# Optimization experiments

Hardware: AMD Instinct MI355X
Metric: run time of the kernel (lower is better)

## Reference

```python
import jax, jax.numpy as jnp
import numpy as np

N_HEADS = 4
N_HIDDEN = 512  # out_features with concat=False
SLOPE = 0.01
NEG = -1e9


def setup_inputs() -> dict:
    key = jax.random.key(0)
    k1, k2, k3, k4 = jax.random.split(key, 4)
    N, F_IN = 8192, 512
    h = jax.random.normal(k1, (N, F_IN), dtype=jnp.float32)
    W = jax.random.normal(k2, (F_IN, N_HIDDEN * N_HEADS), dtype=jnp.float32) * 0.05
    a = jax.random.normal(k3, (N_HEADS, 2 * N_HIDDEN, 1), dtype=jnp.float32) * 0.05
    adj_mat = jnp.where(jax.random.uniform(k4, (N, N)) < 0.01, 0.0, NEG).astype(jnp.float32)
    return {"h": h, "adj_mat": adj_mat, "W": W, "a": a}


def reference(h, adj_mat, W, a):
    N = h.shape[0]
    # [N, H*d] -> [H, N, d]
    ht = (h @ W).reshape(N, N_HEADS, N_HIDDEN).transpose(1, 0, 2)
    a_src = a[:, :N_HIDDEN, 0]   # [H, d]
    a_dst = a[:, N_HIDDEN:, 0]   # [H, d]
    src = jnp.einsum('hnd,hd->hn', ht, a_src)  # [H, N]
    dst = jnp.einsum('hnd,hd->hn', ht, a_dst)  # [H, N]
    # e[h,i,j] = leaky_relu(src[h,i] + dst[h,j]) + adj_mat[i,j]
    e = jax.nn.leaky_relu(src[:, :, None] + dst[:, None, :], SLOPE) + adj_mat[None]
    att = jax.nn.softmax(e, axis=-1)           # [H, N, N]
    h_prime = jnp.einsum('hij,hjd->hid', att, ht)  # [H, N, d]
    return h_prime.mean(axis=0)                # concat=False -> head mean, [N, d]
```

## Files before the change

### kernel.cpp

```cpp
#include <hip/hip_runtime.h>
#include <stdint.h>

#define NN 8192
#define DH 512
#define NH 4
#define LOG2E 1.4426950408889634f

typedef __attribute__((ext_vector_type(8))) short short8;
typedef __attribute__((ext_vector_type(4))) float f32x4;

__device__ __forceinline__ unsigned short f2bf(float f) {
    unsigned int u = __float_as_uint(f);
    unsigned int r = (u + 0x7fffu + ((u >> 16) & 1u)) >> 16;
    return (unsigned short)r;
}

__device__ __forceinline__ void global_to_lds16(const void* g, void* l) {
    __builtin_amdgcn_global_load_lds(
        (const __attribute__((address_space(1))) unsigned int*)g,
        (__attribute__((address_space(3))) unsigned int*)l, 16, 0, 0);
}

__global__ void k_convert_h(const float* __restrict__ hf, unsigned short* __restrict__ hb) {
    const int idx = (blockIdx.x * 256 + threadIdx.x) * 8;
    const float4 f0 = *(const float4*)(hf + idx);
    const float4 f1 = *(const float4*)(hf + idx + 4);
    uint4 o;
    o.x = (unsigned)f2bf(f0.x) | ((unsigned)f2bf(f0.y) << 16);
    o.y = (unsigned)f2bf(f0.z) | ((unsigned)f2bf(f0.w) << 16);
    o.z = (unsigned)f2bf(f1.x) | ((unsigned)f2bf(f1.y) << 16);
    o.w = (unsigned)f2bf(f1.z) | ((unsigned)f2bf(f1.w) << 16);
    *(uint4*)(hb + idx) = o;
}

__global__ void k_transpose_W(const float* __restrict__ W, unsigned short* __restrict__ Wt) {
    __shared__ float t[32][33];
    const int tx = threadIdx.x & 31, ty = threadIdx.x >> 5;
    const int p0 = blockIdx.x * 32, k0 = blockIdx.y * 32;
#pragma unroll
    for (int r = 0; r < 4; r++)
        t[ty + r * 8][tx] = W[(k0 + ty + r * 8) * 2048 + p0 + tx];
    __syncthreads();
#pragma unroll
    for (int r = 0; r < 4; r++)
        Wt[(size_t)(p0 + ty + r * 8) * 512 + k0 + tx] = f2bf(t[tx][ty + r * 8]);
}

__global__ __launch_bounds__(256, 3) void k_gemm(const unsigned short* __restrict__ Wt,
                                                 const unsigned short* __restrict__ hb,
                                                 unsigned short* __restrict__ vt,
                                                 const float* __restrict__ a,
                                                 float* __restrict__ srcL,
                                                 float* __restrict__ dstL) {
    __shared__ alignas(16) char smem[32768];
    const int tid = threadIdx.x;
    const int w = tid >> 6, lane = tid & 63;
    const int lr = lane & 15, lc = lane >> 4;
    const int pBase = blockIdx.y * 128, nBase = blockIdx.x * 128;
    f32x4 acc[4][4] = {};
    const int wr = (w >> 1) * 64, wc = (w & 1) * 64;
    for (int kb = 0; kb < 8; kb++) {
        const int k0 = kb * 64;
#pragma unroll
        for (int it = 0; it < 4; it++) {
            const int o = it * 4096 + w * 1024 + lane * 16;
            const int row = o >> 7;
            const int koff = (o & 127) >> 1;
            global_to_lds16(Wt + (size_t)(pBase + row) * 512 + k0 + koff,
                            smem + it * 4096 + w * 1024);
            global_to_lds16(hb + (size_t)(nBase + row) * 512 + k0 + koff,
                            smem + 16384 + it * 4096 + w * 1024);
        }
        __syncthreads();
#pragma unroll
        for (int kk = 0; kk < 2; kk++) {
            short8 av[4], bv[4];
#pragma unroll
            for (int m = 0; m < 4; m++)
                av[m] = *(const short8*)(smem + (wr + m * 16 + lr) * 128 + kk * 64 + lc * 16);
#pragma unroll
            for (int n = 0; n < 4; n++)
                bv[n] = *(const short8*)(smem + 16384 + (wc + n * 16 + lr) * 128 + kk * 64 + lc * 16);
#pragma unroll
            for (int m = 0; m < 4; m++)
#pragma unroll
                for (int n = 0; n < 4; n++)
                    acc[m][n] = __builtin_amdgcn_mfma_f32_16x16x32_bf16(av[m], bv[n], acc[m][n], 0, 0, 0);
        }
        __syncthreads();
    }
#pragma unroll
    for (int m = 0; m < 4; m++)
#pragma unroll
        for (int n = 0; n < 4; n++)
#pragma unroll
            for (int q = 0; q < 4; q++) {
                const int p = pBase + wr + m * 16 + lc * 4 + q;
                const int ncol = nBase + wc + n * 16 + lr;
                vt[(size_t)p * NN + ncol] = f2bf(acc[m][n][q]);
            }
    const int hh = pBase >> 9;
    const float* __restrict__ ah = a + hh * 1024;
    float ssum[4] = {0.f, 0.f, 0.f, 0.f}, tsum[4] = {0.f, 0.f, 0.f, 0.f};
#pragma unroll
    for (int m = 0; m < 4; m++) {
        const int dbase = (pBase & 511) + wr + m * 16 + lc * 4;
#pragma unroll
        for (int q = 0; q < 4; q++) {
            const float as = ah[dbase + q];
            const float ad = ah[512 + dbase + q];
#pragma unroll
            for (int n = 0; n < 4; n++) {
                ssum[n] += acc[m][n][q] * as;
                tsum[n] += acc[m][n][q] * ad;
            }
        }
    }
#pragma unroll
    for (int n = 0; n < 4; n++) {
        ssum[n] += __shfl_xor(ssum[n], 16, 64);
        ssum[n] += __shfl_xor(ssum[n], 32, 64);
        tsum[n] += __shfl_xor(tsum[n], 16, 64);
        tsum[n] += __shfl_xor(tsum[n], 32, 64);
    }
    if (lane < 16) {
#pragma unroll
        for (int n = 0; n < 4; n++) {
            const int ncol = nBase + wc + n * 16 + lane;
            __hip_atomic_fetch_add(&srcL[hh * NN + ncol], ssum[n] * LOG2E,
                                   __ATOMIC_RELAXED, __HIP_MEMORY_SCOPE_AGENT);
            __hip_atomic_fetch_add(&dstL[hh * NN + ncol], tsum[n] * LOG2E,
                                   __ATOMIC_RELAXED, __HIP_MEMORY_SCOPE_AGENT);
        }
    }
}

#define NJT (NN / 32)
__global__ __launch_bounds__(512, 2) void k_flash(const float* __restrict__ adj,
                                                  const unsigned short* __restrict__ vt,
                                                  const float* __restrict__ srcL,
                                                  const float* __restrict__ dstL,
                                                  float* __restrict__ out) {
    __shared__ alignas(16) char smem[163840];
    char* const vb0 = smem;
    char* const vb1 = smem + 32768;
    char* const vb2 = smem + 65536;
    char* const ab0 = smem + 98304;
    char* const ab1 = smem + 114688;
    char* const ab2 = smem + 131072;
    char* const pb0 = smem + 147456;
    char* const pb1 = smem + 155648;
    float* denom = (float*)(smem + 98304);

    const int tid = threadIdx.x;
    const int w = tid >> 6, lane = tid & 63;
    const int lr = lane & 15, lc = lane >> 4;
    const int h = (int)(blockIdx.x >> 6);
    const int i0 = (int)(blockIdx.x & 63) * 128;
    const int ih = w >> 2, dq = w & 3;

    const int srow = i0 + w * 16 + lr;
    const float srcv = srcL[h * NN + srow];
    const float* __restrict__ dlp = dstL + h * NN + lc * 8;
    const unsigned short* __restrict__ vth = vt + (size_t)(h * 512) * NN;
    float dsum = 0.f;
    f32x4 acc[4][8] = {};

    unsigned voff[4];
#pragma unroll
    for (int it = 0; it < 4; it++) {
        const int o = it * 8192 + w * 1024 + lane * 16;
        const int row = o >> 7;
        const int z = ((o >> 4) & 7) ^ (row & 7);
        const int d = (row << 1) | (z >> 2);
        voff[it] = (unsigned)d * NN + ((z & 3) << 3);
    }
    unsigned aoff[2];
#pragma unroll
    for (int it = 0; it < 2; it++) {
        const int o = it * 8192 + w * 1024 + lane * 16;
        const int row = o >> 7;
        const int hc = ((o >> 4) & 7) ^ (row & 7);
        aoff[it] = (unsigned)(i0 + row) * NN + hc * 4;
    }
    const int rladj = w * 16 + lr;
    const int g1 = (2 * lc) ^ (lr & 7);
    const int ar1 = rladj * 128 + (g1 << 4);
    const int ar2 = rladj * 128 + ((g1 ^ 1) << 4);
    const int prow = w * 16 + lr;
    const int psl = (((prow & 1) << 2) | lc) ^ ((prow >> 1) & 7);
    const int poff = (prow >> 1) * 128 + (psl << 4);

#define STAGE(J0, DST)                                                                   \
    {                                                                                    \
        _Pragma("unroll") for (int it = 0; it < 4; it++)                                 \
            global_to_lds16(vth + voff[it] + (J0), (DST) + it * 8192 + w * 1024);        \
    }

#define STAGE_ADJ(J0, DST)                                                               \
    {                                                                                    \
        _Pragma("unroll") for (int it = 0; it < 2; it++)                                 \
            global_to_lds16(adj + aoff[it] + (J0), (DST) + it * 8192 + w * 1024);        \
    }

#define SCORE(AR_, J0)                                                                   \
    {                                                                                    \
        const float4 aj0 = *(const float4*)((AR_) + ar1);                                \
        const float4 aj1 = *(const float4*)((AR_) + ar2);                                \
        const float padj[8] = {aj0.x, aj0.y, aj0.z, aj0.w, aj1.x, aj1.y, aj1.z, aj1.w};  \
        const float pdst[8] = {dlA0.x, dlA0.y, dlA0.z, dlA0.w,                           \
                               dlA1.x, dlA1.y, dlA1.z, dlA1.w};                          \
        float pv[8];                                                                     \
        _Pragma("unroll") for (int q = 0; q < 8; q++) {                                  \
            const float x = srcv + pdst[q];                                              \
            const float l2 = fmaxf(x, 0.01f * x);                                        \
            float e;                                                                     \
            asm("v_exp_f32 %0, %1" : "=v"(e) : "v"(l2 + padj[q]));                       \
            dsum += e;                                                                   \
            pv[q] = e;                                                                   \
        }                                                                                \
        union { unsigned u[4]; short8 s; } pk;                                           \
        asm("v_cvt_pk_bf16_f32 %0, %1, %2" : "=v"(pk.u[0]) : "v"(pv[0]), "v"(pv[1]));    \
        asm("v_cvt_pk_bf16_f32 %0, %1, %2" : "=v"(pk.u[1]) : "v"(pv[2]), "v"(pv[3]));    \
        asm("v_cvt_pk_bf16_f32 %0, %1, %2" : "=v"(pk.u[2]) : "v"(pv[4]), "v"(pv[5]));    \
        asm("v_cvt_pk_bf16_f32 %0, %1, %2" : "=v"(pk.u[3]) : "v"(pv[6]), "v"(pv[7]));    \
        pfrag = pk.s;                                                                    \
    }

#define PV(VBUF, PBUF)                                                                   \
    {                                                                                    \
        const char* vbp = (VBUF);                                                        \
        const char* pbp = (PBUF);                                                        \
        short8 afr[4];                                                                   \
        _Pragma("unroll") for (int t = 0; t < 4; t++) {                                  \
            const int rr = ih * 64 + t * 16 + lr;                                        \
            const int sl = (((rr & 1) << 2) | lc) ^ ((rr >> 1) & 7);                     \
            afr[t] = *(const short8*)(pbp + (rr >> 1) * 128 + (sl << 4));                \
        }                                                                                \
        __builtin_amdgcn_s_setprio(1);                                                   \
        _Pragma("unroll") for (int s = 0; s < 8; s++) {                                  \
            const int d = dq * 128 + s * 16 + lr;                                        \
            const int sl = (((d & 1) << 2) | lc) ^ ((d >> 1) & 7);                       \
            const short8 bfr = *(const short8*)(vbp + (d >> 1) * 128 + (sl << 4));       \
            _Pragma("unroll") for (int t = 0; t < 4; t++)                                \
                acc[t][s] = __builtin_amdgcn_mfma_f32_16x16x32_bf16(afr[t], bfr,         \
                                                                    acc[t][s], 0, 0, 0); \
        }                                                                                \
        __builtin_amdgcn_s_setprio(0);                                                   \
    }

#define WAITBAR(N)                                                                       \
    asm volatile("s_waitcnt vmcnt(" #N ") lgkmcnt(0)" ::: "memory");                     \
    __builtin_amdgcn_sched_barrier(0);                                                   \
    __builtin_amdgcn_s_barrier();                                                        \
    __builtin_amdgcn_sched_barrier(0);

#define BODY(JB, VC_, VS_, AR_, AS_, PR_, PW_)                       \
    dlA0 = *(const float4*)(dlp + ((JB) + 1) * 32);                  \
    dlA1 = *(const float4*)(dlp + ((JB) + 1) * 32 + 4);              \
    STAGE(((JB) + 1) * 32, VS_);                                     \
    STAGE_ADJ((JB) >= 254 ? 8160 : ((JB) + 2) * 32, AS_);            \
    WAITBAR(8);                                                      \
    PV(VC_, PR_);                                                    \
    SCORE(AR_, ((JB) + 1) * 32);                                     \
    *(short8*)(PW_ + poff) = pfrag;

    float4 dlA0, dlA1;
    short8 pfrag;
    STAGE_ADJ(0, ab0);
    STAGE_ADJ(32, ab1);
    STAGE(0, vb0);
    dlA0 = *(const float4*)(dlp);
    dlA1 = *(const float4*)(dlp + 4);
    WAITBAR(0);
    SCORE(ab0, 0);
    *(short8*)(pb0 + poff) = pfrag;
#pragma unroll 1
    for (int jb = 0; jb < 252; jb += 6) {
        BODY(jb + 0, vb0, vb1, ab1, ab2, pb0, pb1);
        BODY(jb + 1, vb1, vb2, ab2, ab0, pb1, pb0);
        BODY(jb + 2, vb2, vb0, ab0, ab1, pb0, pb1);
        BODY(jb + 3, vb0, vb1, ab1, ab2, pb1, pb0);
        BODY(jb + 4, vb1, vb2, ab2, ab0, pb0, pb1);
        BODY(jb + 5, vb2, vb0, ab0, ab1, pb1, pb0);
    }
    BODY(252, vb0, vb1, ab1, ab2, pb0, pb1);
    BODY(253, vb1, vb2, ab2, ab0, pb1, pb0);
    BODY(254, vb2, vb0, ab0, ab1, pb0, pb1);
    WAITBAR(0);
    PV(vb0, pb1);

    dsum += __shfl_xor(dsum, 16, 64);
    dsum += __shfl_xor(dsum, 32, 64);
    if (lane < 16) denom[w * 16 + lane] = dsum;
    __syncthreads();
#pragma unroll
    for (int t = 0; t < 4; t++) {
        const int rl = ih * 64 + t * 16 + lc * 4;
#pragma unroll
        for (int q = 0; q < 4; q++) {
            const float inv = 0.25f / denom[rl + q];
            float* orow = out + (size_t)(i0 + rl + q) * 512;
#pragma unroll
            for (int s = 0; s < 8; s++) {
                const int d = dq * 128 + s * 16 + lr;
                __hip_atomic_fetch_add(orow + d, acc[t][s][q] * inv,
                                       __ATOMIC_RELAXED, __HIP_MEMORY_SCOPE_AGENT);
            }
        }
    }
}

extern "C" void kernel_launch(void* const* d_in, const int* in_sizes, int n_in,
                              void* d_out, int out_size, void* d_ws, size_t ws_size,
                              hipStream_t stream) {
    const float* h = (const float*)d_in[0];
    const float* adj = (const float*)d_in[1];
    const float* W = (const float*)d_in[2];
    const float* a = (const float*)d_in[3];
    float* out = (float*)d_out;
    char* ws = (char*)d_ws;
    unsigned short* hb = (unsigned short*)ws;
    unsigned short* Wt = (unsigned short*)(ws + 8388608);
    unsigned short* vt = (unsigned short*)(ws + 8388608 + 2097152);
    float* srcL = (float*)(ws + 8388608 + 2097152 + 33554432);
    float* dstL = srcL + NH * NN;

    hipMemsetAsync(d_out, 0, (size_t)out_size * sizeof(float), stream);
    hipMemsetAsync(srcL, 0, 2 * NH * NN * sizeof(float), stream);
    k_convert_h<<<2048, 256, 0, stream>>>(h, hb);
    k_transpose_W<<<dim3(64, 16), 256, 0, stream>>>(W, Wt);
    k_gemm<<<dim3(64, 16), 256, 0, stream>>>(Wt, hb, vt, a, srcL, dstL);
    k_flash<<<256, 512, 0, stream>>>(adj, vt, srcL, dstL, out);
}
```

Baseline: 862.7 us.

## Load adjacency directly to registers and interleave score with split PV MFMAs

Removes the LDS staging of the adjacency tile and instead has each lane read its 8 adjacency values and dst logits straight from global memory into registers one iteration ahead. The PV MFMA loop is split into two halves, with the exp/score computation placed between them so VALU work can overlap matrix work. Shared memory drops from about 160KB to about 113KB. In exchange, the adjacency loads are now less coalesced per wave and their latency must be hidden by the WAITBAR vmcnt accounting, which has not been adjusted.

```diff
diff --git a/kernel.cpp b/kernel.cpp
--- a/kernel.cpp
+++ b/kernel.cpp
@@ -141,16 +141,13 @@
                                                   const float* __restrict__ srcL,
                                                   const float* __restrict__ dstL,
                                                   float* __restrict__ out) {
-    __shared__ alignas(16) char smem[163840];
+    __shared__ alignas(16) char smem[115200];
     char* const vb0 = smem;
     char* const vb1 = smem + 32768;
     char* const vb2 = smem + 65536;
-    char* const ab0 = smem + 98304;
-    char* const ab1 = smem + 114688;
-    char* const ab2 = smem + 131072;
-    char* const pb0 = smem + 147456;
-    char* const pb1 = smem + 155648;
-    float* denom = (float*)(smem + 98304);
+    char* const pb0 = smem + 98304;
+    char* const pb1 = smem + 106496;
+    float* denom = (float*)(smem + 114688);
 
     const int tid = threadIdx.x;
     const int w = tid >> 6, lane = tid & 63;
@@ -161,6 +158,7 @@
 
     const int srow = i0 + w * 16 + lr;
     const float srcv = srcL[h * NN + srow];
+    const float* __restrict__ adjp = adj + (size_t)srow * NN + lc * 8;
     const float* __restrict__ dlp = dstL + h * NN + lc * 8;
     const unsigned short* __restrict__ vth = vt + (size_t)(h * 512) * NN;
     float dsum = 0.f;
@@ -175,18 +173,6 @@
         const int d = (row << 1) | (z >> 2);
         voff[it] = (unsigned)d * NN + ((z & 3) << 3);
     }
-    unsigned aoff[2];
-#pragma unroll
-    for (int it = 0; it < 2; it++) {
-        const int o = it * 8192 + w * 1024 + lane * 16;
-        const int row = o >> 7;
-        const int hc = ((o >> 4) & 7) ^ (row & 7);
-        aoff[it] = (unsigned)(i0 + row) * NN + hc * 4;
-    }
-    const int rladj = w * 16 + lr;
-    const int g1 = (2 * lc) ^ (lr & 7);
-    const int ar1 = rladj * 128 + (g1 << 4);
-    const int ar2 = rladj * 128 + ((g1 ^ 1) << 4);
     const int prow = w * 16 + lr;
     const int psl = (((prow & 1) << 2) | lc) ^ ((prow >> 1) & 7);
     const int poff = (prow >> 1) * 128 + (psl << 4);
@@ -197,48 +183,45 @@
             global_to_lds16(vth + voff[it] + (J0), (DST) + it * 8192 + w * 1024);        \
     }
 
-#define STAGE_ADJ(J0, DST)                                                               \
+#define LOADROW(J0)                                                                      \
+    aj0 = *(const float4*)(adjp + (J0));                                                 \
+    aj1 = *(const float4*)(adjp + (J0) + 4);                                             \
+    dl0 = *(const float4*)(dlp + (J0));                                                  \
+    dl1 = *(const float4*)(dlp + (J0) + 4);
+
+#define SCORE()                                                                          \
     {                                                                                    \
-        _Pragma("unroll") for (int it = 0; it < 2; it++)                                 \
-            global_to_lds16(adj + aoff[it] + (J0), (DST) + it * 8192 + w * 1024);        \
-    }
-
-#define SCORE(AR_, J0)                                                                   \
+        const float padj[8] = {aj0.x, aj0.y, aj0.z, aj0.w, aj1.x, aj1.y, aj1.z, aj1.w};  \
+        const float pdst[8] = {dl0.x, dl0.y, dl0.z, dl0.w, dl1.x, dl1.y, dl1.z, dl1.w};  \
+        union { unsigned u[4]; short8 s; } pk;                                           \
+        _Pragma("unroll") for (int q = 0; q < 4; q++) {                                  \
+            const float xa = srcv + pdst[2 * q];                                         \
+            const float xb = srcv + pdst[2 * q + 1];                                     \
+            const float la = fmaxf(xa, 0.01f * xa) + padj[2 * q];                        \
+            const float lb = fmaxf(xb, 0.01f * xb) + padj[2 * q + 1];                    \
+            float ea, eb;                                                                \
+            asm("v_exp_f32 %0, %1" : "=v"(ea) : "v"(la));                                \
+            asm("v_exp_f32 %0, %1" : "=v"(eb) : "v"(lb));                                \
+            asm("v_cvt_pk_bf16_f32 %0, %1, %2" : "=v"(pk.u[q]) : "v"(ea), "v"(eb));      \
+            dsum += ea + eb;                                                             \
+        }                                                                                \
+        pfrag = pk.s;                                                                    \
+    }
+
+#define AFR(PBUF)                                                                        \
     {                                                                                    \
-        const float4 aj0 = *(const float4*)((AR_) + ar1);                                \
-        const float4 aj1 = *(const float4*)((AR_) + ar2);                                \
-        const float padj[8] = {aj0.x, aj0.y, aj0.z, aj0.w, aj1.x, aj1.y, aj1.z, aj1.w};  \
-        const float pdst[8] = {dlA0.x, dlA0.y, dlA0.z, dlA0.w,                           \
-                               dlA1.x, dlA1.y, dlA1.z, dlA1.w};                          \
-        float pv[8];                                                                     \
-        _Pragma("unroll") for (int q = 0; q < 8; q++) {                                  \
-            const float x = srcv + pdst[q];                                              \
-            const float l2 = fmaxf(x, 0.01f * x);                                        \
-            float e;                                                                     \
-            asm("v_exp_f32 %0, %1" : "=v"(e) : "v"(l2 + padj[q]));                       \
-            dsum += e;                                                                   \
-            pv[q] = e;                                                                   \
-        }                                                                                \
-        union { unsigned u[4]; short8 s; } pk;                                           \
-        asm("v_cvt_pk_bf16_f32 %0, %1, %2" : "=v"(pk.u[0]) : "v"(pv[0]), "v"(pv[1]));    \
-        asm("v_cvt_pk_bf16_f32 %0, %1, %2" : "=v"(pk.u[1]) : "v"(pv[2]), "v"(pv[3]));    \
-        asm("v_cvt_pk_bf16_f32 %0, %1, %2" : "=v"(pk.u[2]) : "v"(pv[4]), "v"(pv[5]));    \
-        asm("v_cvt_pk_bf16_f32 %0, %1, %2" : "=v"(pk.u[3]) : "v"(pv[6]), "v"(pv[7]));    \
-        pfrag = pk.s;                                                                    \
-    }
-
-#define PV(VBUF, PBUF)                                                                   \
-    {                                                                                    \
-        const char* vbp = (VBUF);                                                        \
-        const char* pbp = (PBUF);                                                        \
-        short8 afr[4];                                                                   \
         _Pragma("unroll") for (int t = 0; t < 4; t++) {                                  \
             const int rr = ih * 64 + t * 16 + lr;                                        \
             const int sl = (((rr & 1) << 2) | lc) ^ ((rr >> 1) & 7);                     \
-            afr[t] = *(const short8*)(pbp + (rr >> 1) * 128 + (sl << 4));                \
+            afr[t] = *(const short8*)((PBUF) + (rr >> 1) * 128 + (sl << 4));             \
         }                                                                                \
+    }
+
+#define PVH(VBUF, HALF)                                                                  \
+    {                                                                                    \
+        const char* vbp = (VBUF);                                                        \
         __builtin_amdgcn_s_setprio(1);                                                   \
-        _Pragma("unroll") for (int s = 0; s < 8; s++) {                                  \
+        _Pragma("unroll") for (int s = (HALF) * 4; s < (HALF) * 4 + 4; s++) {            \
             const int d = dq * 128 + s * 16 + lr;                                        \
             const int sl = (((d & 1) << 2) | lc) ^ ((d >> 1) & 7);                       \
             const short8 bfr = *(const short8*)(vbp + (d >> 1) * 128 + (sl << 4));       \
@@ -255,40 +238,40 @@
     __builtin_amdgcn_s_barrier();                                                        \
     __builtin_amdgcn_sched_barrier(0);
 
-#define BODY(JB, VC_, VS_, AR_, AS_, PR_, PW_)                       \
-    dlA0 = *(const float4*)(dlp + ((JB) + 1) * 32);                  \
-    dlA1 = *(const float4*)(dlp + ((JB) + 1) * 32 + 4);              \
-    STAGE(((JB) + 1) * 32, VS_);                                     \
-    STAGE_ADJ((JB) >= 254 ? 8160 : ((JB) + 2) * 32, AS_);            \
-    WAITBAR(8);                                                      \
-    PV(VC_, PR_);                                                    \
-    SCORE(AR_, ((JB) + 1) * 32);                                     \
+#define BODY(JB, VC_, VS_, PR_, PW_)   \
+    LOADROW(((JB) + 1) * 32);          \
+    STAGE(((JB) + 1) * 32, VS_);       \
+    WAITBAR(8);                        \
+    AFR(PR_);                          \
+    PVH(VC_, 0);                       \
+    SCORE();                           \
+    PVH(VC_, 1);                       \
     *(short8*)(PW_ + poff) = pfrag;
 
-    float4 dlA0, dlA1;
+    float4 aj0, aj1, dl0, dl1;
     short8 pfrag;
-    STAGE_ADJ(0, ab0);
-    STAGE_ADJ(32, ab1);
+    short8 afr[4];
+    LOADROW(0);
     STAGE(0, vb0);
-    dlA0 = *(const float4*)(dlp);
-    dlA1 = *(const float4*)(dlp + 4);
     WAITBAR(0);
-    SCORE(ab0, 0);
+    SCORE();
     *(short8*)(pb0 + poff) = pfrag;
 #pragma unroll 1
     for (int jb = 0; jb < 252; jb += 6) {
-        BODY(jb + 0, vb0, vb1, ab1, ab2, pb0, pb1);
-        BODY(jb + 1, vb1, vb2, ab2, ab0, pb1, pb0);
-        BODY(jb + 2, vb2, vb0, ab0, ab1, pb0, pb1);
-        BODY(jb + 3, vb0, vb1, ab1, ab2, pb1, pb0);
-        BODY(jb + 4, vb1, vb2, ab2, ab0, pb0, pb1);
-        BODY(jb + 5, vb2, vb0, ab0, ab1, pb1, pb0);
-    }
-    BODY(252, vb0, vb1, ab1, ab2, pb0, pb1);
-    BODY(253, vb1, vb2, ab2, ab0, pb1, pb0);
-    BODY(254, vb2, vb0, ab0, ab1, pb0, pb1);
+        BODY(jb + 0, vb0, vb1, pb0, pb1);
+        BODY(jb + 1, vb1, vb2, pb1, pb0);
+        BODY(jb + 2, vb2, vb0, pb0, pb1);
+        BODY(jb + 3, vb0, vb1, pb1, pb0);
+        BODY(jb + 4, vb1, vb2, pb0, pb1);
+        BODY(jb + 5, vb2, vb0, pb1, pb0);
+    }
+    BODY(252, vb0, vb1, pb0, pb1);
+    BODY(253, vb1, vb2, pb1, pb0);
+    BODY(254, vb2, vb0, pb0, pb1);
     WAITBAR(0);
-    PV(vb0, pb1);
+    AFR(pb1);
+    PVH(vb0, 0);
+    PVH(vb0, 1);
 
     dsum += __shfl_xor(dsum, 16, 64);
     dsum += __shfl_xor(dsum, 32, 64);
```

After: 858.1 us. About the same (-0.5%).
